# Performance work log

Hardware: AMD Instinct MI355X
Metric: run time of the kernel (lower is better)

## Reference

```python
import jax, jax.numpy as jnp
import numpy as np

ALPHA, BETA, THRESH, T = 0.9, 0.8, 1.0, 10


def _heaviside(x):
    return (x > 0).astype(x.dtype)


def _conv(x, w, b, stride):
    y = jax.lax.conv_general_dilated(
        x, w, window_strides=(stride, stride), padding='VALID',
        dimension_numbers=('NCHW', 'OIHW', 'NCHW'))
    return jax.nn.relu(y + b[None, :, None, None])


def setup_inputs() -> dict:
    key = jax.random.key(0)
    ks = jax.random.split(key, 16)
    B = 128
    state = jax.random.uniform(ks[0], (B, 3, 224, 224), dtype=jnp.float32)
    history = jax.random.uniform(ks[1], (B, 90), dtype=jnp.float32)
    fc_in = 64 * 24 * 24 + 90  # 36954

    def w(k, shape, fan_in):
        return jax.random.normal(k, shape, dtype=jnp.float32) * (1.0 / np.sqrt(fan_in))

    return {
        'state': state, 'history': history,
        'cw1': w(ks[2], (32, 3, 8, 8), 3 * 8 * 8), 'cb1': jnp.zeros((32,), jnp.float32),
        'cw2': w(ks[3], (64, 32, 4, 4), 32 * 4 * 4), 'cb2': jnp.zeros((64,), jnp.float32),
        'cw3': w(ks[4], (64, 64, 3, 3), 64 * 3 * 3), 'cb3': jnp.zeros((64,), jnp.float32),
        'w1': w(ks[5], (128, fc_in), fc_in), 'b1': jnp.zeros((128,), jnp.float32),
        'w2': w(ks[6], (256, 128), 128), 'b2': jnp.zeros((256,), jnp.float32),
        'w3': w(ks[7], (9, 256), 256), 'b3': jnp.zeros((9,), jnp.float32),
    }


def reference(state, history, cw1, cb1, cw2, cb2, cw3, cb3, w1, b1, w2, b2, w3, b3):
    B = state.shape[0]
    f = _conv(state, cw1, cb1, 4)
    f = _conv(f, cw2, cb2, 2)
    f = _conv(f, cw3, cb3, 1)
    x = jnp.concatenate([f.reshape(B, -1), history], axis=1)  # (B, 36954)
    # encoding='constant' -> input (hence h1) is identical every timestep
    h1 = x @ w1.T + b1  # (B,128)

    def lif(h, mem, syn):
        new_syn = ALPHA * syn + h
        new_mem = BETA * mem + new_syn
        out = _heaviside(new_mem - THRESH)
        return out, new_mem - out * THRESH, new_syn

    z = lambda d: jnp.zeros((B, d), x.dtype)
    carry0 = (z(128), z(128), z(256), z(256), z(9), z(9), z(9))

    def step(carry, _):
        mem1, syn1, mem2, syn2, mem3, syn3, pot = carry
        spk1, mem1, syn1 = lif(h1, mem1, syn1)
        h2 = spk1 @ w2.T + b2
        spk2, mem2, syn2 = lif(h2, mem2, syn2)
        h3 = spk2 @ w3.T + b3
        syn3 = ALPHA * syn3 + h3
        mem3 = BETA * mem3 + syn3
        pot = pot + mem3
        return (mem1, syn1, mem2, syn2, mem3, syn3, pot), None

    carry, _ = jax.lax.scan(step, carry0, None, length=T)
    return carry[6] / T
```

## Files before the change

kernel.cpp:

```cpp
#include <hip/hip_runtime.h>

#define ALPHA 0.9f
#define BETA  0.8f
#define XS 36960

typedef _Float16 f16;
typedef _Float16 f16x8 __attribute__((ext_vector_type(8)));
typedef float f32x4 __attribute__((ext_vector_type(4)));


__global__ __launch_bounds__(256) void prep_weights_kernel(
    const float* __restrict__ cw1, const float* __restrict__ cw2,
    const float* __restrict__ cw3, const float* __restrict__ w2,
    f16* __restrict__ w1h, f16* __restrict__ w1l,
    f16* __restrict__ w2h, f16* __restrict__ w2l,
    f16* __restrict__ w3h, f16* __restrict__ w3l,
    float* __restrict__ w2q) {
  int i = blockIdx.x * 256 + threadIdx.x;
  if (i < 6144)  { float v = cw1[i]; f16 h = (f16)v; w1h[i] = h; w1l[i] = (f16)(v - (float)h); }
  if (i < 32768) { float v = cw2[i]; f16 h = (f16)v; w2h[i] = h; w2l[i] = (f16)(v - (float)h); }
  if (i < 49152) {
    int oc = i / 768, r = i % 768;
    int c = r / 12, rr = r % 12, kh = rr >> 2, kw = rr & 3;
    float v = (kw < 3) ? cw3[oc * 576 + c * 9 + kh * 3 + kw] : 0.f;
    f16 h = (f16)v; w3h[i] = h; w3l[i] = (f16)(v - (float)h);
  }
  if (i < 32768) {
    int j = i >> 7, k = i & 127;
    w2q[((k >> 2) * 256 + j) * 4 + (k & 3)] = w2[i];
  }
}

__global__ __launch_bounds__(256) void pad_w1_kernel(
    const float* __restrict__ w1, float* __restrict__ w1p) {
  int i = blockIdx.x * 256 + threadIdx.x;
  if (i < 128 * 18480) {
    int j = i / 18480, c = i - j * 18480;
    float2 v;
    if (c < 18477) v = *(const float2*)&w1[(size_t)j * 36954 + c * 2];
    else v = make_float2(0.f, 0.f);
    *(float2*)&w1p[(size_t)j * XS + c * 2] = v;
  }
}

template<int IC, int KH, int KWP, int KWV, int S, int IH, int IW,
         int OW, int OHW, int OC, int NPB, bool OUT_X>
__global__ __launch_bounds__(256) void mfma_conv_kernel(
    const float* __restrict__ in, const f16* __restrict__ wh,
    const f16* __restrict__ wl, const float* __restrict__ bias,
    float* __restrict__ out) {
  constexpr int K = IC * KH * KWP;
  constexpr int KCH = K / 32;
  constexpr int MTILES = OC / 16;
  constexpr int NTILES = NPB / 16;
  constexpr int WOC = MTILES / 2;
  constexpr int ASLOTS = OC * 4;
  constexpr int BSLOTS = NPB * 4;
  constexpr int SITER = BSLOTS / 256;
  __shared__ f16 Ah[MTILES * 512], Al[MTILES * 512];
  __shared__ f16 Bh[NTILES * 512], Bl[NTILES * 512];

  const int n = blockIdx.y;
  const int pos0 = blockIdx.x * NPB;
  const int t = threadIdx.x;
  const int w = t >> 6, lane = t & 63, quad = lane >> 4, l16 = lane & 15;
  const int woc  = (WOC == 1) ? 0 : (w & 1);
  const int wpos = (WOC == 1) ? w : (w >> 1);
  const size_t in_n = (size_t)n * IC * IH * IW;

  int ohS[SITER], owS[SITER], kq8[SITER];
#pragma unroll
  for (int si = 0; si < SITER; ++si) {
    int s = t + si * 256;
    int nt = s >> 6, prem = s & 15;
    int pos = pos0 + nt * 16 + prem;
    if (pos > OHW - 1) pos = OHW - 1;
    int oh = pos / OW, ow = pos - oh * OW;
    ohS[si] = oh * S; owS[si] = ow * S;
    kq8[si] = ((s >> 4) & 3) * 8;
  }
  const int am = (t >> 6) * 16 + (t & 15);
  const int ak = ((t >> 4) & 3) * 8;

  f32x4 acc[2][2] = {};

  for (int kt = 0; kt < KCH; ++kt) {
    __syncthreads();
    if (t < ASLOTS) {
      *(f16x8*)&Ah[t * 8] = *(const f16x8*)&wh[am * K + kt * 32 + ak];
      *(f16x8*)&Al[t * 8] = *(const f16x8*)&wl[am * K + kt * 32 + ak];
    }
#pragma unroll
    for (int si = 0; si < SITER; ++si) {
      int s = t + si * 256;
      int kb = kt * 32 + kq8[si];
      f16x8 bh, bl;
#pragma unroll
      for (int half = 0; half < 2; ++half) {
        int kk = kb + half * 4;
        int kw0 = kk & (KWP - 1);
        int row = kk / KWP;
        int c = row / KH, kh = row - c * KH;
        const float* p = in + in_n +
            ((size_t)c * IH + ohS[si] + kh) * IW + owS[si] + kw0;
#pragma unroll
        for (int e = 0; e < 4; ++e) {
          float v = (KWV < KWP && e >= KWV) ? 0.f : p[e];
          f16 h = (f16)v;
          bh[half * 4 + e] = h;
          bl[half * 4 + e] = (f16)(v - (float)h);
        }
      }
      *(f16x8*)&Bh[s * 8] = bh;
      *(f16x8*)&Bl[s * 8] = bl;
    }
    __syncthreads();
    f16x8 ah0 = *(const f16x8*)&Ah[(woc * 2 + 0) * 512 + lane * 8];
    f16x8 ah1 = *(const f16x8*)&Ah[(woc * 2 + 1) * 512 + lane * 8];
    f16x8 al0 = *(const f16x8*)&Al[(woc * 2 + 0) * 512 + lane * 8];
    f16x8 al1 = *(const f16x8*)&Al[(woc * 2 + 1) * 512 + lane * 8];
    f16x8 bh0 = *(const f16x8*)&Bh[(wpos * 2 + 0) * 512 + lane * 8];
    f16x8 bh1 = *(const f16x8*)&Bh[(wpos * 2 + 1) * 512 + lane * 8];
    f16x8 bl0 = *(const f16x8*)&Bl[(wpos * 2 + 0) * 512 + lane * 8];
    f16x8 bl1 = *(const f16x8*)&Bl[(wpos * 2 + 1) * 512 + lane * 8];
    acc[0][0] = __builtin_amdgcn_mfma_f32_16x16x32_f16(ah0, bh0, acc[0][0], 0, 0, 0);
    acc[0][0] = __builtin_amdgcn_mfma_f32_16x16x32_f16(ah0, bl0, acc[0][0], 0, 0, 0);
    acc[0][0] = __builtin_amdgcn_mfma_f32_16x16x32_f16(al0, bh0, acc[0][0], 0, 0, 0);
    acc[1][0] = __builtin_amdgcn_mfma_f32_16x16x32_f16(ah1, bh0, acc[1][0], 0, 0, 0);
    acc[1][0] = __builtin_amdgcn_mfma_f32_16x16x32_f16(ah1, bl0, acc[1][0], 0, 0, 0);
    acc[1][0] = __builtin_amdgcn_mfma_f32_16x16x32_f16(al1, bh0, acc[1][0], 0, 0, 0);
    acc[0][1] = __builtin_amdgcn_mfma_f32_16x16x32_f16(ah0, bh1, acc[0][1], 0, 0, 0);
    acc[0][1] = __builtin_amdgcn_mfma_f32_16x16x32_f16(ah0, bl1, acc[0][1], 0, 0, 0);
    acc[0][1] = __builtin_amdgcn_mfma_f32_16x16x32_f16(al0, bh1, acc[0][1], 0, 0, 0);
    acc[1][1] = __builtin_amdgcn_mfma_f32_16x16x32_f16(ah1, bh1, acc[1][1], 0, 0, 0);
    acc[1][1] = __builtin_amdgcn_mfma_f32_16x16x32_f16(ah1, bl1, acc[1][1], 0, 0, 0);
    acc[1][1] = __builtin_amdgcn_mfma_f32_16x16x32_f16(al1, bh1, acc[1][1], 0, 0, 0);
  }
#pragma unroll
  for (int mtl = 0; mtl < 2; ++mtl)
#pragma unroll
    for (int ntl = 0; ntl < 2; ++ntl)
#pragma unroll
      for (int r = 0; r < 4; ++r) {
        int oc  = (woc * 2 + mtl) * 16 + quad * 4 + r;
        int pos = pos0 + (wpos * 2 + ntl) * 16 + l16;
        if (pos < OHW) {
          float v = acc[mtl][ntl][r] + bias[oc];
          v = v > 0.f ? v : 0.f;
          if (OUT_X)
            out[(size_t)n * XS + oc * OHW + pos] = v;
          else
            out[((size_t)n * OC + oc) * OHW + pos] = v;
        }
      }
}

__global__ __launch_bounds__(256) void histpack_kernel(
    const float* __restrict__ h, float* __restrict__ x) {
  int i = blockIdx.x * 256 + threadIdx.x;
  if (i < 128 * 96) {
    int n = i / 96, k = i % 96;
    x[(size_t)n * XS + 36864 + k] = (k < 90) ? h[n * 90 + k] : 0.f;
  }
}

#define FC1_KT 289
__global__ __launch_bounds__(256) void fc1_kernel(
    const float* __restrict__ x, const float* __restrict__ w1p,
    float* __restrict__ P) {
  int kt = blockIdx.x;
  int t  = threadIdx.x;
  int bq = t & 15, jq = t >> 4;
  __shared__ float xs[128 * 36];
  __shared__ float wsm[128 * 36];
  float acc[8][8];
#pragma unroll
  for (int bb = 0; bb < 8; ++bb)
#pragma unroll
    for (int jj = 0; jj < 8; ++jj) acc[bb][jj] = 0.f;

  int cs = t & 7;
  int rs = t >> 3;
#pragma unroll 1
  for (int s = 0; s < 4; ++s) {
    int k0 = kt * 128 + s * 32;
    __syncthreads();
#pragma unroll
    for (int p = 0; p < 4; ++p) {
      int r = rs + p * 32;
      int gk = k0 + cs * 4;
      float4 xv, wv;
      if (gk < 36954) {
        xv = *(const float4*)&x[(size_t)r * XS + gk];
        wv = *(const float4*)&w1p[(size_t)r * XS + gk];
      } else {
        xv = make_float4(0.f, 0.f, 0.f, 0.f);
        wv = make_float4(0.f, 0.f, 0.f, 0.f);
      }
      *(float4*)&xs[r * 36 + cs * 4] = xv;
      *(float4*)&wsm[r * 36 + cs * 4] = wv;
    }
    __syncthreads();
#pragma unroll 1
    for (int kk = 0; kk < 32; kk += 4) {
      float4 xv[8], wv[8];
#pragma unroll
      for (int i = 0; i < 8; ++i)
        xv[i] = *(const float4*)&xs[(bq + 16 * i) * 36 + kk];
#pragma unroll
      for (int i = 0; i < 8; ++i)
        wv[i] = *(const float4*)&wsm[(jq + 16 * i) * 36 + kk];
#pragma unroll
      for (int bb = 0; bb < 8; ++bb)
#pragma unroll
        for (int jj = 0; jj < 8; ++jj) {
          acc[bb][jj] = fmaf(xv[bb].x, wv[jj].x, acc[bb][jj]);
          acc[bb][jj] = fmaf(xv[bb].y, wv[jj].y, acc[bb][jj]);
          acc[bb][jj] = fmaf(xv[bb].z, wv[jj].z, acc[bb][jj]);
          acc[bb][jj] = fmaf(xv[bb].w, wv[jj].w, acc[bb][jj]);
        }
    }
  }
  float* Pb = P + (size_t)kt * 16384;
#pragma unroll
  for (int bb = 0; bb < 8; ++bb)
#pragma unroll
    for (int jj = 0; jj < 8; ++jj)
      Pb[(bq + 16 * bb) * 128 + jq + 16 * jj] = acc[bb][jj];
}

__global__ __launch_bounds__(256) void reduce_p_kernel(
    const float* __restrict__ P, const float* __restrict__ b1,
    float* __restrict__ h1s) {
  int idx = blockIdx.x * 256 + threadIdx.x;
  int j = idx & 127;
  float a0 = 0.f, a1 = 0.f, a2 = 0.f, a3 = 0.f;
  int kt = 0;
#pragma unroll 2
  for (; kt + 3 < FC1_KT; kt += 4) {
    a0 += P[(size_t)(kt + 0) * 16384 + idx];
    a1 += P[(size_t)(kt + 1) * 16384 + idx];
    a2 += P[(size_t)(kt + 2) * 16384 + idx];
    a3 += P[(size_t)(kt + 3) * 16384 + idx];
  }
  for (; kt < FC1_KT; ++kt) a0 += P[(size_t)kt * 16384 + idx];
  h1s[idx] = ((a0 + a1) + (a2 + a3)) + b1[j];
}

__global__ __launch_bounds__(256, 1) void recur_kernel(
    const float* __restrict__ h1s,
    const float4* __restrict__ w2q,
    const float* __restrict__ b2,
    const float* __restrict__ w3,
    const float* __restrict__ b3,
    float* __restrict__ out) {
  int b = blockIdx.x;
  int t = threadIdx.x;
  __shared__ float spk1s[128];
  __shared__ float spk2s[256];
  __shared__ float w3s[9 * 256];
  __shared__ float part[9][16];
  float4 w2c[32];
#pragma unroll
  for (int k4 = 0; k4 < 32; ++k4) w2c[k4] = w2q[k4 * 256 + t];
  for (int i = t; i < 9 * 256; i += 256) w3s[i] = w3[i];
  float h1 = (t < 128) ? h1s[b * 128 + t] : 0.f;
  float mem1 = 0.f, syn1 = 0.f, mem2 = 0.f, syn2 = 0.f;
  float b2v = b2[t];
  float mem3 = 0.f, syn3 = 0.f, pot = 0.f;
  float b3v = (t < 9) ? b3[t] : 0.f;
  int j3 = t >> 4, p = t & 15;
  __syncthreads();

  for (int step = 0; step < 10; ++step) {
    if (t < 128) {
      syn1 = ALPHA * syn1 + h1;
      mem1 = BETA * mem1 + syn1;
      float s = (mem1 > 1.0f) ? 1.0f : 0.0f;
      mem1 -= s;
      spk1s[t] = s;
    }
    __syncthreads();
    float h2 = b2v;
#pragma unroll
    for (int k4 = 0; k4 < 32; ++k4) {
      float4 s = *(const float4*)&spk1s[k4 * 4];
      h2 = fmaf(s.x, w2c[k4].x, h2);
      h2 = fmaf(s.y, w2c[k4].y, h2);
      h2 = fmaf(s.z, w2c[k4].z, h2);
      h2 = fmaf(s.w, w2c[k4].w, h2);
    }
    syn2 = ALPHA * syn2 + h2;
    mem2 = BETA * mem2 + syn2;
    float s2 = (mem2 > 1.0f) ? 1.0f : 0.0f;
    mem2 -= s2;
    spk2s[t] = s2;
    __syncthreads();
    if (t < 144) {
      float a = 0.f;
      const float* wr = &w3s[j3 * 256 + p * 16];
      const float* sp = &spk2s[p * 16];
#pragma unroll
      for (int e = 0; e < 16; ++e) a = fmaf(sp[e], wr[e], a);
      part[j3][p] = a;
    }
    __syncthreads();
    if (t < 9) {
      float a = b3v;
#pragma unroll
      for (int p2 = 0; p2 < 16; ++p2) a += part[t][p2];
      syn3 = ALPHA * syn3 + a;
      mem3 = BETA * mem3 + syn3;
      pot += mem3;
    }
  }
  if (t < 9) out[b * 9 + t] = pot * 0.1f;
}

extern "C" void kernel_launch(void* const* d_in, const int* in_sizes, int n_in,
                              void* d_out, int out_size, void* d_ws, size_t ws_size,
                              hipStream_t stream) {
  const float* state   = (const float*)d_in[0];
  const float* history = (const float*)d_in[1];
  const float* cw1 = (const float*)d_in[2];
  const float* cb1 = (const float*)d_in[3];
  const float* cw2 = (const float*)d_in[4];
  const float* cb2 = (const float*)d_in[5];
  const float* cw3 = (const float*)d_in[6];
  const float* cb3 = (const float*)d_in[7];
  const float* w1  = (const float*)d_in[8];
  const float* b1  = (const float*)d_in[9];
  const float* w2  = (const float*)d_in[10];
  const float* b2  = (const float*)d_in[11];
  const float* w3  = (const float*)d_in[12];
  const float* b3  = (const float*)d_in[13];
  float* out = (float*)d_out;
  char* ws = (char*)d_ws;

  float* f1  = (float*)(ws + 0);
  float* xb  = (float*)(ws + 0);
  float* w1p = (float*)(ws + 18923520);
  float* f2  = (float*)(ws + 49561600);
  float* P   = (float*)(ws + 49561600);
  f16* wf1h = (f16*)(ws + 71712768);
  f16* wf1l = (f16*)(ws + 71725056);
  f16* wf2h = (f16*)(ws + 71737344);
  f16* wf2l = (f16*)(ws + 71802880);
  f16* wf3h = (f16*)(ws + 71868416);
  f16* wf3l = (f16*)(ws + 71966720);
  float* w2q = (float*)(ws + 72065024);
  float* h1s = (float*)(ws + 72196096);

  prep_weights_kernel<<<192, 256, 0, stream>>>(cw1, cw2, cw3, w2,
                                               wf1h, wf1l, wf2h, wf2l,
                                               wf3h, wf3l, w2q);
  mfma_conv_kernel<3, 8, 8, 8, 4, 224, 224, 55, 3025, 32, 128, false>
      <<<dim3(24, 128), 256, 0, stream>>>(state, wf1h, wf1l, cb1, f1);
  mfma_conv_kernel<32, 4, 4, 4, 2, 55, 55, 26, 676, 64, 64, false>
      <<<dim3(11, 128), 256, 0, stream>>>(f1, wf2h, wf2l, cb2, f2);
  pad_w1_kernel<<<9240, 256, 0, stream>>>(w1, w1p);
  mfma_conv_kernel<64, 3, 4, 3, 1, 26, 26, 24, 576, 64, 64, true>
      <<<dim3(9, 128), 256, 0, stream>>>(f2, wf3h, wf3l, cb3, xb);
  histpack_kernel<<<48, 256, 0, stream>>>(history, xb);
  fc1_kernel<<<FC1_KT, 256, 0, stream>>>(xb, w1p, P);
  reduce_p_kernel<<<64, 256, 0, stream>>>(P, b1, h1s);
  recur_kernel<<<128, 256, 0, stream>>>(h1s, (const float4*)w2q, b2, w3, b3, out);
}
```

Before: 346.9 us.

## Double-buffer conv LDS tiles and prefetch next K-chunk into registers

Conv MFMA kernel now keeps two LDS buffers and prefetches the next K-chunk's weights and input patches into registers while the current chunk computes. This removes one barrier per iteration and hides global load latency behind MFMA work. Input reads become float4 vector loads that may be unaligned and read an extra padded element for the 3-wide case. LDS usage and register pressure increase.

After: 348.5 us. Within noise of the previous version (+0.4%).

```diff
diff --git a/kernel.cpp b/kernel.cpp
--- a/kernel.cpp
+++ b/kernel.cpp
@@ -57,8 +57,8 @@
   constexpr int ASLOTS = OC * 4;
   constexpr int BSLOTS = NPB * 4;
   constexpr int SITER = BSLOTS / 256;
-  __shared__ f16 Ah[MTILES * 512], Al[MTILES * 512];
-  __shared__ f16 Bh[NTILES * 512], Bl[NTILES * 512];
+  __shared__ f16 Ah[2][MTILES * 512], Al[2][MTILES * 512];
+  __shared__ f16 Bh[2][NTILES * 512], Bl[2][NTILES * 512];
 
   const int n = blockIdx.y;
   const int pos0 = blockIdx.x * NPB;
@@ -83,46 +83,70 @@
   const int ak = ((t >> 4) & 3) * 8;
 
   f32x4 acc[2][2] = {};
-
-  for (int kt = 0; kt < KCH; ++kt) {
-    __syncthreads();
-    if (t < ASLOTS) {
-      *(f16x8*)&Ah[t * 8] = *(const f16x8*)&wh[am * K + kt * 32 + ak];
-      *(f16x8*)&Al[t * 8] = *(const f16x8*)&wl[am * K + kt * 32 + ak];
-    }
-#pragma unroll
-    for (int si = 0; si < SITER; ++si) {
-      int s = t + si * 256;
-      int kb = kt * 32 + kq8[si];
-      f16x8 bh, bl;
+  float4 pv[SITER][2];
+  f16x8 pah = {}, pal = {};
+
+  auto loadB = [&](int kt) {
+#pragma unroll
+    for (int si = 0; si < SITER; ++si)
 #pragma unroll
       for (int half = 0; half < 2; ++half) {
-        int kk = kb + half * 4;
+        int kk = kt * 32 + kq8[si] + half * 4;
         int kw0 = kk & (KWP - 1);
         int row = kk / KWP;
         int c = row / KH, kh = row - c * KH;
-        const float* p = in + in_n +
-            ((size_t)c * IH + ohS[si] + kh) * IW + owS[si] + kw0;
+        pv[si][half] = *(const float4*)(in + in_n +
+            ((size_t)c * IH + ohS[si] + kh) * IW + owS[si] + kw0);
+      }
+  };
+
+  loadB(0);
+  if (t < ASLOTS) {
+    pah = *(const f16x8*)&wh[am * K + ak];
+    pal = *(const f16x8*)&wl[am * K + ak];
+  }
+
+  for (int kt = 0; kt < KCH; ++kt) {
+    const int cur = kt & 1;
+    if (t < ASLOTS) {
+      *(f16x8*)&Ah[cur][t * 8] = pah;
+      *(f16x8*)&Al[cur][t * 8] = pal;
+    }
+#pragma unroll
+    for (int si = 0; si < SITER; ++si) {
+      int s = t + si * 256;
+      f16x8 bh, bl;
+#pragma unroll
+      for (int half = 0; half < 2; ++half) {
+        float pe[4] = {pv[si][half].x, pv[si][half].y,
+                       pv[si][half].z, pv[si][half].w};
 #pragma unroll
         for (int e = 0; e < 4; ++e) {
-          float v = (KWV < KWP && e >= KWV) ? 0.f : p[e];
+          float v = (KWV < KWP && e >= KWV) ? 0.f : pe[e];
           f16 h = (f16)v;
           bh[half * 4 + e] = h;
           bl[half * 4 + e] = (f16)(v - (float)h);
         }
       }
-      *(f16x8*)&Bh[s * 8] = bh;
-      *(f16x8*)&Bl[s * 8] = bl;
-    }
-    __syncthreads();
-    f16x8 ah0 = *(const f16x8*)&Ah[(woc * 2 + 0) * 512 + lane * 8];
-    f16x8 ah1 = *(const f16x8*)&Ah[(woc * 2 + 1) * 512 + lane * 8];
-    f16x8 al0 = *(const f16x8*)&Al[(woc * 2 + 0) * 512 + lane * 8];
-    f16x8 al1 = *(const f16x8*)&Al[(woc * 2 + 1) * 512 + lane * 8];
-    f16x8 bh0 = *(const f16x8*)&Bh[(wpos * 2 + 0) * 512 + lane * 8];
-    f16x8 bh1 = *(const f16x8*)&Bh[(wpos * 2 + 1) * 512 + lane * 8];
-    f16x8 bl0 = *(const f16x8*)&Bl[(wpos * 2 + 0) * 512 + lane * 8];
-    f16x8 bl1 = *(const f16x8*)&Bl[(wpos * 2 + 1) * 512 + lane * 8];
+      *(f16x8*)&Bh[cur][s * 8] = bh;
+      *(f16x8*)&Bl[cur][s * 8] = bl;
+    }
+    if (kt + 1 < KCH) {
+      loadB(kt + 1);
+      if (t < ASLOTS) {
+        pah = *(const f16x8*)&wh[am * K + (kt + 1) * 32 + ak];
+        pal = *(const f16x8*)&wl[am * K + (kt + 1) * 32 + ak];
+      }
+    }
+    __syncthreads();
+    f16x8 ah0 = *(const f16x8*)&Ah[cur][(woc * 2 + 0) * 512 + lane * 8];
+    f16x8 ah1 = *(const f16x8*)&Ah[cur][(woc * 2 + 1) * 512 + lane * 8];
+    f16x8 al0 = *(const f16x8*)&Al[cur][(woc * 2 + 0) * 512 + lane * 8];
+    f16x8 al1 = *(const f16x8*)&Al[cur][(woc * 2 + 1) * 512 + lane * 8];
+    f16x8 bh0 = *(const f16x8*)&Bh[cur][(wpos * 2 + 0) * 512 + lane * 8];
+    f16x8 bh1 = *(const f16x8*)&Bh[cur][(wpos * 2 + 1) * 512 + lane * 8];
+    f16x8 bl0 = *(const f16x8*)&Bl[cur][(wpos * 2 + 0) * 512 + lane * 8];
+    f16x8 bl1 = *(const f16x8*)&Bl[cur][(wpos * 2 + 1) * 512 + lane * 8];
     acc[0][0] = __builtin_amdgcn_mfma_f32_16x16x32_f16(ah0, bh0, acc[0][0], 0, 0, 0);
     acc[0][0] = __builtin_amdgcn_mfma_f32_16x16x32_f16(ah0, bl0, acc[0][0], 0, 0, 0);
     acc[0][0] = __builtin_amdgcn_mfma_f32_16x16x32_f16(al0, bh0, acc[0][0], 0, 0, 0);
```
